# Performance work log

Measured on AMD Instinct MI355X. Metric: run time of the kernel, lower is better.

Reference implementation:

```python
import jax, jax.numpy as jnp
import numpy as np

LAMBDA_PROTO = 0.5
EPS = 1e-12  # F.normalize eps


def setup_inputs() -> dict:
    key = jax.random.key(0)
    k1, k2, k3 = jax.random.split(key, 3)
    N, D, C = 262144, 128, 64
    emb = jax.random.normal(k1, (N, D), dtype=jnp.float32)
    logits = jax.random.normal(k2, (N, C), dtype=jnp.float32)
    labels = jax.random.randint(k3, (N,), 0, C, dtype=jnp.int64)
    return {"emb": emb, "logits": logits, "labels": labels}


def reference(emb, logits, labels):
    N, D = emb.shape
    C = logits.shape[1]

    # F.normalize(emb, dim=1): x / max(||x||, eps)
    nrm = jnp.sqrt(jnp.sum(emb * emb, axis=1, keepdims=True))
    z = emb / jnp.maximum(nrm, EPS)

    # Cross-entropy (mean reduction, no class weights)
    logp = jax.nn.log_softmax(logits, axis=-1)
    ce = -jnp.mean(jnp.take_along_axis(logp, labels[:, None], axis=1))

    # Per-class stats via segment reduce (single fused pass, no python loop)
    lab = labels.astype(jnp.int32)
    counts = jax.ops.segment_sum(jnp.ones((N,), jnp.float32), lab, num_segments=C)  # [C]
    sums = jax.ops.segment_sum(z, lab, num_segments=C)                               # [C, D]
    sq = jax.ops.segment_sum(jnp.sum(z * z, axis=1), lab, num_segments=C)            # [C]

    safe_n = jnp.maximum(counts, 1.0)
    mu = sums / safe_n[:, None]
    # sum_i ||z_i - mu||^2 = sum_i ||z_i||^2 - n * ||mu||^2
    ssd = sq - counts * jnp.sum(mu * mu, axis=1)
    per_class = ssd / safe_n  # mean over samples of squared distance

    valid = counts > 1.0  # classes with <=1 sample are skipped
    n_valid = jnp.sum(valid.astype(jnp.float32))
    proto_loss = jnp.sum(jnp.where(valid, per_class, 0.0)) / jnp.maximum(n_valid, 1.0)

    return (1.0 - LAMBDA_PROTO) * ce + LAMBDA_PROTO * proto_loss
```

## Files before the change

kernel.cpp:

```cpp
#include <hip/hip_runtime.h>
#include <math.h>

#define N_ROWS 262144
#define D 128
#define C 64
#define HB 512
#define CSTRIDE 4608
#define FB 1024
#define FT 512
#define TMAX 9
#define OCTW 132

#define OFF_HIST   0
#define OFF_BASES  (HB * C)
#define OFF_IDX    (2 * HB * C)
#define OFF_CNT    (2 * HB * C + C * CSTRIDE)
#define OFF_CEB    (OFF_CNT + C)
#define OFF_OCT    (OFF_CEB + FB)
#define OFF_RES    (OFF_OCT + FB * OCTW)

__device__ __forceinline__ void gload8(float4& a, float4& b, const float* p) {
  asm volatile("global_load_dwordx4 %0, %2, off\n\t"
               "global_load_dwordx4 %1, %2, off offset:16"
               : "=&v"(a), "=&v"(b)
               : "v"(p));
}

__global__ __launch_bounds__(256) void hist_kernel(
    const int* __restrict__ labels, int* __restrict__ hist) {
  __shared__ int sH[C];
  const int tid = threadIdx.x;
  if (tid < C) sH[tid] = 0;
  __syncthreads();
  const int2 l = *(const int2*)(labels + blockIdx.x * 512 + tid * 2);
  atomicAdd(&sH[l.x], 1);
  atomicAdd(&sH[l.y], 1);
  __syncthreads();
  if (tid < C) hist[blockIdx.x * C + tid] = sH[tid];
}

__global__ __launch_bounds__(256) void scan_kernel(
    const int* __restrict__ hist, int* __restrict__ bases,
    int* __restrict__ cnts) {
  __shared__ int sA[256], sB[256];
  const int c = blockIdx.x, t = threadIdx.x;
  const int h0 = hist[(2 * t) * C + c];
  const int h1 = hist[(2 * t + 1) * C + c];
  const int tot = h0 + h1;
  sA[t] = tot;
  __syncthreads();
#pragma unroll
  for (int st = 0; st < 8; ++st) {
    const int off = 1 << st;
    if (st & 1) sA[t] = sB[t] + ((t >= off) ? sB[t - off] : 0);
    else        sB[t] = sA[t] + ((t >= off) ? sA[t - off] : 0);
    __syncthreads();
  }
  const int incl = sA[t];
  const int excl = incl - tot;
  bases[(2 * t) * C + c] = excl;
  bases[(2 * t + 1) * C + c] = excl + h0;
  if (t == 255) cnts[c] = incl;
}

__global__ __launch_bounds__(512) void scatter_kernel(
    const int* __restrict__ labels, const int* __restrict__ bases,
    int* __restrict__ idx) {
  __shared__ int sCur[C];
  const int t = threadIdx.x, b = blockIdx.x;
  if (t < C) sCur[t] = bases[b * C + t];
  __syncthreads();
  const int row = b * 512 + t;
  const int lab = labels[row];
  const int pos = atomicAdd(&sCur[lab], 1);
  idx[lab * CSTRIDE + pos] = row;
}

__global__ __launch_bounds__(FT, 4) void fused_kernel(
    const float* __restrict__ emb, const float* __restrict__ logits,
    const int* __restrict__ labels, const int* __restrict__ idxArr,
    const int* __restrict__ cnts, float* __restrict__ ceB,
    float* __restrict__ oct) {
  __shared__ float sCe[8];
  __shared__ float sR[8][OCTW];

  const int tid = threadIdx.x;
  const int wave = tid >> 6, lane = tid & 63;
  const int g = lane >> 4, lp = lane & 15;
  const int b = blockIdx.x;

  auto ce_phase = [&]() {
    const int rowBase = b * 256 + wave * 32 + g;
    float ce_acc = 0.f;
    float4 tA, tB;
    int labA = 0, labB = 0;
    tA = *(const float4*)(logits + (size_t)rowBase * C + lp * 4);
    labA = labels[rowBase];
    tB = tA;
#pragma unroll
    for (int it = 0; it < 8; ++it) {
      const float4 t4 = (it & 1) ? tB : tA;
      const int lab = (it & 1) ? labB : labA;
      if (it + 1 < 8) {
        const int row = rowBase + (it + 1) * 4;
        if (it & 1) {
          tA = *(const float4*)(logits + (size_t)row * C + lp * 4);
          labA = labels[row];
        } else {
          tB = *(const float4*)(logits + (size_t)row * C + lp * 4);
          labB = labels[row];
        }
      }
      float p = __expf(t4.x) + __expf(t4.y) + __expf(t4.z) + __expf(t4.w);
      float tl = 0.f;
      if ((lab >> 2) == lp) {
        const int k = lab & 3;
        tl = k == 0 ? t4.x : k == 1 ? t4.y : k == 2 ? t4.z : t4.w;
      }
      p += __shfl_xor(p, 1);  tl += __shfl_xor(tl, 1);
      p += __shfl_xor(p, 2);  tl += __shfl_xor(tl, 2);
      p += __shfl_xor(p, 4);  tl += __shfl_xor(tl, 4);
      p += __shfl_xor(p, 8);  tl += __shfl_xor(tl, 8);
      if (lp == 0) ce_acc += __logf(p) - tl;
    }
    ce_acc += __shfl_xor(ce_acc, 16);
    ce_acc += __shfl_xor(ce_acc, 32);
    if (lane == 0) sCe[wave] = ce_acc;
    __syncthreads();
    if (tid == 0) {
      float s = 0.f;
#pragma unroll
      for (int w = 0; w < 8; ++w) s += sCe[w];
      ceB[b] = s;
    }
  };

  auto proto_phase = [&]() {
    const int c = b >> 4, o = b & 15;
    const int gg = o * 32 + wave * 4 + g;
    const int n = cnts[c];
    const int nm1 = (n > 0) ? n - 1 : 0;
    const int* ip = idxArr + c * CSTRIDE;

    int rI[TMAX];
#pragma unroll
    for (int t = 0; t < TMAX; ++t) {
      const int e = gg + 512 * t;
      rI[t] = ip[e < nm1 ? e : nm1];
    }
#pragma unroll
    for (int t = 0; t < TMAX; ++t) asm volatile("" :: "v"(rI[t]));
    __builtin_amdgcn_sched_barrier(0);

    float4 s0a, s0b, s1a, s1b, s2a, s2b, s3a, s3b, s4a, s4b, s5a, s5b;
    gload8(s0a, s0b, emb + (size_t)rI[0] * D + lp * 8);
    gload8(s1a, s1b, emb + (size_t)rI[1] * D + lp * 8);
    gload8(s2a, s2b, emb + (size_t)rI[2] * D + lp * 8);
    gload8(s3a, s3b, emb + (size_t)rI[3] * D + lp * 8);
    gload8(s4a, s4b, emb + (size_t)rI[4] * D + lp * 8);
    gload8(s5a, s5b, emb + (size_t)rI[5] * D + lp * 8);

    float4 accA = {0.f, 0.f, 0.f, 0.f}, accB = {0.f, 0.f, 0.f, 0.f};
    float cnt = 0.f, sq = 0.f;

    auto consume = [&](const float4 ea, const float4 eb, const int t) {
      float ss = ea.x * ea.x + ea.y * ea.y + ea.z * ea.z + ea.w * ea.w +
                 eb.x * eb.x + eb.y * eb.y + eb.z * eb.z + eb.w * eb.w;
      ss += __shfl_xor(ss, 1);
      ss += __shfl_xor(ss, 2);
      ss += __shfl_xor(ss, 4);
      ss += __shfl_xor(ss, 8);
      const float inv = 1.0f / fmaxf(sqrtf(ss), 1e-12f);
      const bool valid = (gg + 512 * t) < n;
      const float sc = valid ? inv : 0.f;
      accA.x += ea.x * sc;  accA.y += ea.y * sc;
      accA.z += ea.z * sc;  accA.w += ea.w * sc;
      accB.x += eb.x * sc;  accB.y += eb.y * sc;
      accB.z += eb.z * sc;  accB.w += eb.w * sc;
      if (lp == 0) {
        cnt += valid ? 1.f : 0.f;
        sq += valid ? ss * inv * inv : 0.f;
      }
    };

#define PSTEP(T, NW, SA, SB)                            \
    asm volatile("s_waitcnt vmcnt(" #NW ")");           \
    __builtin_amdgcn_sched_barrier(0);                  \
    consume(SA, SB, T);

    PSTEP(0, 10, s0a, s0b)  gload8(s0a, s0b, emb + (size_t)rI[6] * D + lp * 8);
    PSTEP(1, 10, s1a, s1b)  gload8(s1a, s1b, emb + (size_t)rI[7] * D + lp * 8);
    PSTEP(2, 10, s2a, s2b)  gload8(s2a, s2b, emb + (size_t)rI[8] * D + lp * 8);
    PSTEP(3, 10, s3a, s3b)
    PSTEP(4, 8,  s4a, s4b)
    PSTEP(5, 6,  s5a, s5b)
    PSTEP(6, 4,  s0a, s0b)
    PSTEP(7, 2,  s1a, s1b)
    PSTEP(8, 0,  s2a, s2b)
#undef PSTEP

#pragma unroll
    for (int off = 16; off <= 32; off <<= 1) {
      accA.x += __shfl_xor(accA.x, off);  accA.y += __shfl_xor(accA.y, off);
      accA.z += __shfl_xor(accA.z, off);  accA.w += __shfl_xor(accA.w, off);
      accB.x += __shfl_xor(accB.x, off);  accB.y += __shfl_xor(accB.y, off);
      accB.z += __shfl_xor(accB.z, off);  accB.w += __shfl_xor(accB.w, off);
      cnt += __shfl_xor(cnt, off);
      sq += __shfl_xor(sq, off);
    }

    if (lane < 16) {
      *(float4*)&sR[wave][lp * 8] = accA;
      *(float4*)&sR[wave][lp * 8 + 4] = accB;
    }
    if (lane == 0) { sR[wave][128] = cnt; sR[wave][129] = sq; }
    __syncthreads();
    if (tid < 130) {
      float s = 0.f;
#pragma unroll
      for (int w = 0; w < 8; ++w) s += sR[w][tid];
      oct[(size_t)b * OCTW + tid] = s;
    }
  };

  if (b & 1) { ce_phase(); __syncthreads(); proto_phase(); }
  else       { proto_phase(); __syncthreads(); ce_phase(); }
}

__global__ __launch_bounds__(128) void class_kernel(
    const float* __restrict__ oct, float* __restrict__ res) {
  __shared__ float sM[2];
  const int c = blockIdx.x, t = threadIdx.x;
  float s = 0.f, n = 0.f, sq = 0.f;
#pragma unroll
  for (int o = 0; o < 16; ++o) {
    const float* f = oct + (size_t)(c * 16 + o) * OCTW;
    s += f[t];
    n += f[128];
    sq += f[129];
  }
  const float safe = fmaxf(n, 1.f);
  const float mu = s / safe;
  float msq = mu * mu;
#pragma unroll
  for (int off = 1; off < 64; off <<= 1) msq += __shfl_xor(msq, off);
  if ((t & 63) == 0) sM[t >> 6] = msq;
  __syncthreads();
  if (t == 0) {
    const float ssd = sq - n * (sM[0] + sM[1]);
    const bool valid = n > 1.f;
    res[c] = valid ? ssd / safe : 0.f;
    res[C + c] = valid ? 1.f : 0.f;
  }
}

__global__ __launch_bounds__(256) void final_kernel(
    const float* __restrict__ ceB, const float* __restrict__ res,
    float* __restrict__ out) {
  __shared__ float sv[4][3];
  const int tid = threadIdx.x, wave = tid >> 6, lane = tid & 63;
  float ce = 0.f;
  for (int i = tid; i < FB; i += 256) ce += ceB[i];
  float pr = 0.f, nv = 0.f;
  if (wave == 0) { pr = res[lane]; nv = res[C + lane]; }
#pragma unroll
  for (int off = 1; off < 64; off <<= 1) {
    ce += __shfl_xor(ce, off);
    pr += __shfl_xor(pr, off);
    nv += __shfl_xor(nv, off);
  }
  if (lane == 0) { sv[wave][0] = ce; sv[wave][1] = pr; sv[wave][2] = nv; }
  __syncthreads();
  if (tid == 0) {
    const float c2 = sv[0][0] + sv[1][0] + sv[2][0] + sv[3][0];
    const float p2 = sv[0][1] + sv[1][1] + sv[2][1] + sv[3][1];
    const float n2 = sv[0][2] + sv[1][2] + sv[2][2] + sv[3][2];
    out[0] = 0.5f * (c2 / (float)N_ROWS) + 0.5f * (p2 / fmaxf(n2, 1.f));
  }
}

extern "C" void kernel_launch(void* const* d_in, const int* in_sizes, int n_in,
                              void* d_out, int out_size, void* d_ws, size_t ws_size,
                              hipStream_t stream) {
  const float* emb = (const float*)d_in[0];
  const float* logits = (const float*)d_in[1];
  const int* labels = (const int*)d_in[2];
  int* wsi = (int*)d_ws;
  float* wsf = (float*)d_ws;
  float* out = (float*)d_out;

  int* hist = wsi + OFF_HIST;
  int* bases = wsi + OFF_BASES;
  int* idx = wsi + OFF_IDX;
  int* cnts = wsi + OFF_CNT;
  float* ceB = wsf + OFF_CEB;
  float* oct = wsf + OFF_OCT;
  float* res = wsf + OFF_RES;

  hist_kernel<<<HB, 256, 0, stream>>>(labels, hist);
  scan_kernel<<<C, 256, 0, stream>>>(hist, bases, cnts);
  scatter_kernel<<<HB, 512, 0, stream>>>(labels, bases, idx);
  fused_kernel<<<FB, FT, 0, stream>>>(emb, logits, labels, idx, cnts, ceB, oct);
  class_kernel<<<C, 128, 0, stream>>>(oct, res);
  final_kernel<<<1, 256, 0, stream>>>(ceB, res, out);
}
```

Baseline: 54.13 us.

## Merge histogram, scan and scatter into one atomic-reservation build kernel

Replaces the three-kernel counting sort (per-block histogram, per-class scan, scatter) with a memset plus a single build kernel. Each block computes local per-class offsets with shared atomics, then reserves a global range per class with one atomicAdd on the class counters. This removes two kernel launches and the intermediate hist/bases buffers. In exchange, the row order within each class becomes nondeterministic, which can slightly change the float summation order downstream.

Result: faster. 52.97 us (-2.1%).

```diff
diff --git a/kernel.cpp b/kernel.cpp
--- a/kernel.cpp
+++ b/kernel.cpp
@@ -4,17 +4,15 @@
 #define N_ROWS 262144
 #define D 128
 #define C 64
-#define HB 512
 #define CSTRIDE 4608
+#define BB 64
 #define FB 1024
 #define FT 512
 #define TMAX 9
 #define OCTW 132
 
-#define OFF_HIST   0
-#define OFF_BASES  (HB * C)
-#define OFF_IDX    (2 * HB * C)
-#define OFF_CNT    (2 * HB * C + C * CSTRIDE)
+#define OFF_IDX    0
+#define OFF_CNT    (C * CSTRIDE)
 #define OFF_CEB    (OFF_CNT + C)
 #define OFF_OCT    (OFF_CEB + FB)
 #define OFF_RES    (OFF_OCT + FB * OCTW)
@@ -26,54 +24,27 @@
                : "v"(p));
 }
 
-__global__ __launch_bounds__(256) void hist_kernel(
-    const int* __restrict__ labels, int* __restrict__ hist) {
+__global__ __launch_bounds__(1024) void build_kernel(
+    const int* __restrict__ labels, int* __restrict__ idx,
+    int* __restrict__ cnts) {
   __shared__ int sH[C];
-  const int tid = threadIdx.x;
-  if (tid < C) sH[tid] = 0;
-  __syncthreads();
-  const int2 l = *(const int2*)(labels + blockIdx.x * 512 + tid * 2);
-  atomicAdd(&sH[l.x], 1);
-  atomicAdd(&sH[l.y], 1);
-  __syncthreads();
-  if (tid < C) hist[blockIdx.x * C + tid] = sH[tid];
-}
-
-__global__ __launch_bounds__(256) void scan_kernel(
-    const int* __restrict__ hist, int* __restrict__ bases,
-    int* __restrict__ cnts) {
-  __shared__ int sA[256], sB[256];
-  const int c = blockIdx.x, t = threadIdx.x;
-  const int h0 = hist[(2 * t) * C + c];
-  const int h1 = hist[(2 * t + 1) * C + c];
-  const int tot = h0 + h1;
-  sA[t] = tot;
-  __syncthreads();
-#pragma unroll
-  for (int st = 0; st < 8; ++st) {
-    const int off = 1 << st;
-    if (st & 1) sA[t] = sB[t] + ((t >= off) ? sB[t - off] : 0);
-    else        sB[t] = sA[t] + ((t >= off) ? sA[t - off] : 0);
-    __syncthreads();
-  }
-  const int incl = sA[t];
-  const int excl = incl - tot;
-  bases[(2 * t) * C + c] = excl;
-  bases[(2 * t + 1) * C + c] = excl + h0;
-  if (t == 255) cnts[c] = incl;
-}
-
-__global__ __launch_bounds__(512) void scatter_kernel(
-    const int* __restrict__ labels, const int* __restrict__ bases,
-    int* __restrict__ idx) {
-  __shared__ int sCur[C];
+  __shared__ int sBase[C];
   const int t = threadIdx.x, b = blockIdx.x;
-  if (t < C) sCur[t] = bases[b * C + t];
-  __syncthreads();
-  const int row = b * 512 + t;
-  const int lab = labels[row];
-  const int pos = atomicAdd(&sCur[lab], 1);
-  idx[lab * CSTRIDE + pos] = row;
+  if (t < C) sH[t] = 0;
+  __syncthreads();
+  const int row = b * 4096 + t * 4;
+  const int4 l = *(const int4*)(labels + row);
+  const int p0 = atomicAdd(&sH[l.x], 1);
+  const int p1 = atomicAdd(&sH[l.y], 1);
+  const int p2 = atomicAdd(&sH[l.z], 1);
+  const int p3 = atomicAdd(&sH[l.w], 1);
+  __syncthreads();
+  if (t < C) sBase[t] = atomicAdd(&cnts[t], sH[t]);
+  __syncthreads();
+  idx[l.x * CSTRIDE + sBase[l.x] + p0] = row;
+  idx[l.y * CSTRIDE + sBase[l.y] + p1] = row + 1;
+  idx[l.z * CSTRIDE + sBase[l.z] + p2] = row + 2;
+  idx[l.w * CSTRIDE + sBase[l.w] + p3] = row + 3;
 }
 
 __global__ __launch_bounds__(FT, 4) void fused_kernel(
@@ -183,9 +154,9 @@
       }
     };
 
-#define PSTEP(T, NW, SA, SB)                            \
-    asm volatile("s_waitcnt vmcnt(" #NW ")");           \
-    __builtin_amdgcn_sched_barrier(0);                  \
+#define PSTEP(T, NW, SA, SB)                          \
+    asm volatile("s_waitcnt vmcnt(" #NW ")");         \
+    __builtin_amdgcn_sched_barrier(0);                \
     consume(SA, SB, T);
 
     PSTEP(0, 10, s0a, s0b)  gload8(s0a, s0b, emb + (size_t)rI[6] * D + lp * 8);
@@ -289,17 +260,14 @@
   float* wsf = (float*)d_ws;
   float* out = (float*)d_out;
 
-  int* hist = wsi + OFF_HIST;
-  int* bases = wsi + OFF_BASES;
   int* idx = wsi + OFF_IDX;
   int* cnts = wsi + OFF_CNT;
   float* ceB = wsf + OFF_CEB;
   float* oct = wsf + OFF_OCT;
   float* res = wsf + OFF_RES;
 
-  hist_kernel<<<HB, 256, 0, stream>>>(labels, hist);
-  scan_kernel<<<C, 256, 0, stream>>>(hist, bases, cnts);
-  scatter_kernel<<<HB, 512, 0, stream>>>(labels, bases, idx);
+  hipMemsetAsync(cnts, 0, C * sizeof(int), stream);
+  build_kernel<<<BB, 1024, 0, stream>>>(labels, idx, cnts);
   fused_kernel<<<FB, FT, 0, stream>>>(emb, logits, labels, idx, cnts, ceB, oct);
   class_kernel<<<C, 128, 0, stream>>>(oct, res);
   final_kernel<<<1, 256, 0, stream>>>(ceB, res, out);
```
